# Kernel tuning notes

Hardware: AMD Instinct MI355X
Metric: run time of the kernel (lower is better)

## Reference

```python
import jax, jax.numpy as jnp
import numpy as np

EPS = 1e-6
DELTA = 1e-6
GAMMA = 1.0


def setup_inputs() -> dict:
    key = jax.random.key(0)
    ks = jax.random.split(key, 6)
    B, N, D, DDIR, DSIM = 2, 384, 256, 128, 64
    sc = lambda d: 1.0 / np.sqrt(d)
    return {
        "t": jax.random.normal(ks[0], (B, N, D), jnp.float32),
        "Qd": jax.random.normal(ks[1], (D, DDIR), jnp.float32) * sc(D),
        "Kd": jax.random.normal(ks[2], (D, DDIR), jnp.float32) * sc(D),
        "Vd": jax.random.normal(ks[3], (DDIR, D), jnp.float32) * sc(DDIR),
        "Qs": jax.random.normal(ks[4], (D, DSIM), jnp.float32) * sc(D),
        "Ks": jax.random.normal(ks[5], (D, DSIM), jnp.float32) * sc(D),
        "a_l": jnp.ones((1,), jnp.float32),
        "b_l": jnp.zeros((1,), jnp.float32),
    }


def reference(t, Qd, Kd, Vd, Qs, Ks, a_l, b_l):
    B, N, D = t.shape
    d_sim = Qs.shape[1]
    # --- similarity: s_ij = <Qs t_i, Ks t_j>/sqrt(d_sim), then symmetrize ---
    q = t @ Qs  # (B,N,d_sim)
    k = t @ Ks
    s = jnp.einsum('bnd,bmd->bnm', q, k) / jnp.sqrt(jnp.float32(d_sim))
    s = 0.5 * (s + s.transpose(0, 2, 1))
    # --- global z-score over off-diagonal entries (biased var) ---
    eye = jnp.eye(N, dtype=bool)[None]  # (1,N,N)
    cnt = jnp.float32(N * (N - 1))
    mu = jnp.where(eye, 0.0, s).sum((1, 2), keepdims=True) / cnt  # (B,1,1)
    var = jnp.where(eye, 0.0, (s - mu) ** 2).sum((1, 2), keepdims=True) / cnt
    s_hat = (s - mu) / jnp.sqrt(var + EPS)
    tilde_s = a_l.reshape(-1, 1, 1) * s_hat + b_l.reshape(-1, 1, 1)
    # --- gates / mass / inertia / apportioned step ---
    A = jax.nn.sigmoid(tilde_s)                                  # (B,N,N)
    m = 1.0 / (jnp.exp(GAMMA * tilde_s).sum(axis=2) + EPS)       # (B,N)
    w = A * m[:, None, :]                                        # w_ij = m_j A_ij
    alpha = A * (w / (w.sum(axis=2, keepdims=True) + DELTA))     # (B,N,N)
    # --- antisymmetric Hadamard direction gate ---
    qd = t @ Qd  # (B,N,d_dir)
    kd = t @ Kd
    had = qd[:, :, None, :] * kd[:, None, :, :]                  # (B,N,N,d_dir)
    kappa = jnp.einsum('bijr,rd->bijd', had, Vd)                 # (B,N,N,D)
    gate = jax.nn.sigmoid(kappa - kappa.transpose(0, 2, 1, 3))
    Dpair = gate * (t[:, :, None, :] - t[:, None, :, :])         # D_ij = gate*(t_i - t_j)
    # --- exclude self pairs, aggregate update ---
    off = ~eye  # (1,N,N)
    alpha = jnp.where(off, alpha, 0.0)
    Dpair = jnp.where(off[..., None], Dpair, 0.0)
    t_next = t - jnp.einsum('bnm,bnmd->bnd', alpha, Dpair)
    return t_next
```

## Files before the change

### kernel.cpp

```cpp
#include <hip/hip_runtime.h>

#define Bn 2
#define Nn 384
#define Dn 256
#define Rn 128
#define Sn 64
#define BNn (Bn*Nn)
#define NEG_LOG2E -1.44269504088896f

typedef short short8 __attribute__((ext_vector_type(8)));
typedef float f32x4 __attribute__((ext_vector_type(4)));
typedef unsigned int uint;
typedef unsigned short ushort;

static __device__ __forceinline__ float fast_sigmoid(float x) {
    return __builtin_amdgcn_rcpf(1.0f + __expf(-x));
}
static __device__ __forceinline__ ushort f2bf(float f) {
    uint u = __float_as_uint(f);
    uint r = (u + 0x7fffu + ((u >> 16) & 1u)) >> 16;
    return (ushort)r;
}
static __device__ __forceinline__ float bf2f(ushort u) {
    return __uint_as_float(((uint)u) << 16);
}

__global__ __launch_bounds__(256)
void prep_kernel(const float* __restrict__ t,
                 const float* __restrict__ Qd, const float* __restrict__ Kd,
                 const float* __restrict__ Vd,
                 const float* __restrict__ Qs, const float* __restrict__ Ks,
                 float* __restrict__ q, float* __restrict__ k,
                 ushort* __restrict__ qdb, ushort* __restrict__ kdb,
                 ushort* __restrict__ VdT, float* __restrict__ stats) {
    const int bi = blockIdx.x;
    const int tid = threadIdx.x;
    if (bi >= BNn) {
        const int idx = (bi - BNn) * 256 + tid;
        const int d = idx >> 7, r = idx & 127;
        VdT[idx] = f2bf(NEG_LOG2E * Vd[(size_t)r * Dn + d]);
        if (bi == BNn && tid < 4) stats[tid] = 0.0f;
        return;
    }
    __shared__ float trow[Dn];
    trow[tid] = t[(size_t)bi * Dn + tid];
    __syncthreads();
    {
        const float* W = (tid < 128) ? Qd : Kd;
        ushort* ob = (tid < 128) ? qdb : kdb;
        const int col = tid & 127;
        float a0 = 0.f;
        for (int kk = 0; kk < Dn; kk += 4) {
            float4 tv = *(const float4*)&trow[kk];
            a0 += tv.x * W[(size_t)(kk + 0) * 128 + col]
                + tv.y * W[(size_t)(kk + 1) * 128 + col]
                + tv.z * W[(size_t)(kk + 2) * 128 + col]
                + tv.w * W[(size_t)(kk + 3) * 128 + col];
        }
        ob[(size_t)bi * 128 + col] = f2bf(a0);
    }
    if (tid < 128) {
        const float* W = (tid < 64) ? Qs : Ks;
        float* of = (tid < 64) ? q : k;
        const int col = tid & 63;
        float a0 = 0.f;
        for (int kk = 0; kk < Dn; kk += 4) {
            float4 tv = *(const float4*)&trow[kk];
            a0 += tv.x * W[(size_t)(kk + 0) * 64 + col]
                + tv.y * W[(size_t)(kk + 1) * 64 + col]
                + tv.z * W[(size_t)(kk + 2) * 64 + col]
                + tv.w * W[(size_t)(kk + 3) * 64 + col];
        }
        of[(size_t)bi * 64 + col] = a0;
    }
}

__global__ __launch_bounds__(256)
void ssym_kernel(const float* __restrict__ q, const float* __restrict__ k,
                 float* __restrict__ ssym, float* __restrict__ stats) {
    __shared__ float qi[16][68], ki[16][68], qj[16][68], kj[16][68];
    __shared__ float part[8];
    const int b = blockIdx.z, it = blockIdx.x, jt = blockIdx.y;
    const int tid = threadIdx.x;
    const int r0 = tid >> 6, c = tid & 63;
#pragma unroll
    for (int p = 0; p < 4; ++p) {
        int row = r0 + 4 * p;
        qi[row][c] = q[((size_t)(b * Nn + it * 16 + row)) * Sn + c];
        ki[row][c] = k[((size_t)(b * Nn + it * 16 + row)) * Sn + c];
        qj[row][c] = q[((size_t)(b * Nn + jt * 16 + row)) * Sn + c];
        kj[row][c] = k[((size_t)(b * Nn + jt * 16 + row)) * Sn + c];
    }
    __syncthreads();
    const int ti = tid >> 4, tj = tid & 15;
    float acc = 0.0f;
#pragma unroll
    for (int dd = 0; dd < Sn; dd += 4) {
        float4 a  = *(const float4*)&qi[ti][dd];
        float4 bb = *(const float4*)&kj[tj][dd];
        float4 cc = *(const float4*)&qj[tj][dd];
        float4 d  = *(const float4*)&ki[ti][dd];
        acc += a.x * bb.x + a.y * bb.y + a.z * bb.z + a.w * bb.w
             + cc.x * d.x + cc.y * d.y + cc.z * d.z + cc.w * d.w;
    }
    const float sval = acc * 0.0625f;
    const int gi = it * 16 + ti, gj = jt * 16 + tj;
    ssym[((size_t)(b * Nn + gi)) * Nn + gj] = sval;
    const float v = (gi == gj) ? 0.0f : sval;

    float vs = v, v2 = v * v;
#pragma unroll
    for (int mask = 32; mask > 0; mask >>= 1) {
        vs += __shfl_xor(vs, mask);
        v2 += __shfl_xor(v2, mask);
    }
    const int lane = tid & 63, wave = tid >> 6;
    if (lane == 0) { part[wave] = vs; part[4 + wave] = v2; }
    __syncthreads();
    if (tid == 0) {
        atomicAdd(&stats[b * 2 + 0], part[0] + part[1] + part[2] + part[3]);
        atomicAdd(&stats[b * 2 + 1], part[4] + part[5] + part[6] + part[7]);
    }
}

__global__ __launch_bounds__(256)
void m_kernel(const float* __restrict__ ssym, const float* __restrict__ stats,
              const float* __restrict__ a_l, const float* __restrict__ b_l,
              float* __restrict__ m) {
    __shared__ float part[4];
    const int row = blockIdx.x;
    const int b = row / Nn;
    const float cnt_inv = 1.0f / (float)(Nn * (Nn - 1));
    const float mu = stats[b * 2 + 0] * cnt_inv;
    const float var = stats[b * 2 + 1] * cnt_inv - mu * mu;
    const float isg = rsqrtf(var + 1e-6f);
    const float a = a_l[0], bbias = b_l[0];
    const int tid = threadIdx.x;
    float sum = __expf(a * (ssym[(size_t)row * Nn + tid] - mu) * isg + bbias);
    if (tid < 128)
        sum += __expf(a * (ssym[(size_t)row * Nn + 256 + tid] - mu) * isg + bbias);
#pragma unroll
    for (int mask = 32; mask > 0; mask >>= 1) sum += __shfl_xor(sum, mask);
    if ((tid & 63) == 0) part[tid >> 6] = sum;
    __syncthreads();
    if (tid == 0) m[row] = 1.0f / (part[0] + part[1] + part[2] + part[3] + 1e-6f);
}

__global__ __launch_bounds__(256, 4)
void pair_kernel(const float* __restrict__ t, const float* __restrict__ ssym,
                 const float* __restrict__ mptr, const float* __restrict__ stats,
                 const float* __restrict__ a_l, const float* __restrict__ b_l,
                 const ushort* __restrict__ qdb, const ushort* __restrict__ kdb,
                 const ushort* __restrict__ VdT, float* __restrict__ out) {
    __shared__ ushort qs_lds[2][4096];
    __shared__ ushort ks_lds[2][4096];
    __shared__ float alpha_s[Nn];
    __shared__ float part[4];

    const int blk = blockIdx.x;
    const int bi = blk >> 2;
    const int dq = blk & 3;
    const int b = bi / Nn;
    const int i = bi - b * Nn;
    const int tid = threadIdx.x;
    const int wave = tid >> 6, lane = tid & 63;
    const int ln = lane & 15, quad = lane >> 4;
    const int wd0 = dq * 64 + wave * 16;

    {
        const float cnt_inv = 1.0f / (float)(Nn * (Nn - 1));
        const float mu = stats[b * 2 + 0] * cnt_inv;
        const float var = stats[b * 2 + 1] * cnt_inv - mu * mu;
        const float isg = rsqrtf(var + 1e-6f);
        const float a = a_l[0], bbias = b_l[0];
        float A0, am0, A1 = 0.f, am1 = 0.f;
        {
            float s0 = ssym[(size_t)bi * Nn + tid];
            A0 = fast_sigmoid(a * (s0 - mu) * isg + bbias);
            am0 = A0 * mptr[b * Nn + tid];
        }
        if (tid < 128) {
            float s1 = ssym[(size_t)bi * Nn + 256 + tid];
            A1 = fast_sigmoid(a * (s1 - mu) * isg + bbias);
            am1 = A1 * mptr[b * Nn + 256 + tid];
        }
        float sum = am0 + am1;
#pragma unroll
        for (int mask = 32; mask > 0; mask >>= 1) sum += __shfl_xor(sum, mask);
        if (lane == 0) part[wave] = sum;
        __syncthreads();
        const float inv = 1.0f / (part[0] + part[1] + part[2] + part[3] + 1e-6f);
        alpha_s[tid] = (tid == i) ? 0.f : A0 * am0 * inv;
        if (tid < 128)
            alpha_s[256 + tid] = ((256 + tid) == i) ? 0.f : A1 * am1 * inv;
    }

    short8 uf[4], wf[4];
    {
        const size_t qrow = (size_t)bi * Rn;
#pragma unroll
        for (int ks = 0; ks < 4; ++ks) {
            short8 qv = *(const short8*)&qdb[qrow + ks * 32 + quad * 8];
            short8 kv = *(const short8*)&kdb[qrow + ks * 32 + quad * 8];
            short8 vv = *(const short8*)&VdT[(size_t)(wd0 + ln) * Rn + ks * 32 + quad * 8];
            short8 uu, ww;
#pragma unroll
            for (int e = 0; e < 8; ++e) {
                float vf_ = bf2f((ushort)vv[e]);
                uu[e] = (short)f2bf(vf_ * bf2f((ushort)qv[e]));
                ww[e] = (short)f2bf(vf_ * bf2f((ushort)kv[e]));
            }
            uf[ks] = uu;
            wf[ks] = ww;
        }
    }

    float4 tiv = *(const float4*)&t[(size_t)bi * Dn + wd0 + quad * 4];
    float4 outac = make_float4(0.f, 0.f, 0.f, 0.f);

    const ushort* qsrc = qdb + (size_t)b * Nn * Rn;
    const ushort* ksrc = kdb + (size_t)b * Nn * Rn;
    const float* tbase_ = t + (size_t)b * Nn * Dn + wd0 + quad * 4;

    const int jr = tid >> 4;
    const int ch = tid & 15;
    const int wb = (ch >> 2) * 1024 + (ch & 3) * 256 + ((jr ^ (ch & 7)) * 16);

    uint4 sq0, sq1, sk0, sk1;

    {
        const ushort* q0 = qsrc + (size_t)jr * Rn + ch * 8;
        const ushort* k0 = ksrc + (size_t)jr * Rn + ch * 8;
        sq0 = *(const uint4*)q0;  sq1 = *(const uint4*)(q0 + 16 * Rn);
        sk0 = *(const uint4*)k0;  sk1 = *(const uint4*)(k0 + 16 * Rn);
        *(uint4*)((char*)&qs_lds[0][0] + wb)        = sq0;
        *(uint4*)((char*)&qs_lds[0][0] + wb + 4096) = sq1;
        *(uint4*)((char*)&ks_lds[0][0] + wb)        = sk0;
        *(uint4*)((char*)&ks_lds[0][0] + wb + 4096) = sk1;
    }
    __syncthreads();

    const int lane_off = ((ln ^ quad) * 16) + quad * 256;

    float4 tj_cur = *(const float4*)&tbase_[(size_t)ln * Dn];

    int cur = 0;
#pragma unroll 1
    for (int tt = 0; tt < Nn / 32; ++tt) {
        const int tn = (tt + 1 < Nn / 32) ? tt + 1 : 0;
        {
            const ushort* q0 = qsrc + (size_t)(tn * 32 + jr) * Rn + ch * 8;
            const ushort* k0 = ksrc + (size_t)(tn * 32 + jr) * Rn + ch * 8;
            sq0 = *(const uint4*)q0;  sq1 = *(const uint4*)(q0 + 16 * Rn);
            sk0 = *(const uint4*)k0;  sk1 = *(const uint4*)(k0 + 16 * Rn);
        }

        const char* qbuf = (const char*)&qs_lds[cur][0];
        const char* kbuf = (const char*)&ks_lds[cur][0];

#pragma unroll
        for (int s = 0; s < 2; ++s) {
            const int jj = tt * 2 + s;
            const int jn = (jj + 1 < Nn / 16) ? jj + 1 : 0;
            float4 tj_nxt = *(const float4*)&tbase_[(size_t)(jn * 16 + ln) * Dn];

            f32x4 accU = {0.f, 0.f, 0.f, 0.f}, accW = {0.f, 0.f, 0.f, 0.f};
#pragma unroll
            for (int ks = 0; ks < 4; ++ks) {
                const int off = s * 4096 + ks * 1024 + (lane_off ^ ((ks & 1) << 6));
                short8 bk = *(const short8*)(kbuf + off);
                short8 bq = *(const short8*)(qbuf + off);
                accU = __builtin_amdgcn_mfma_f32_16x16x32_bf16(uf[ks], bk, accU, 0, 0, 0);
                accW = __builtin_amdgcn_mfma_f32_16x16x32_bf16(wf[ks], bq, accW, 0, 0, 0);
            }
            const float al = alpha_s[jj * 16 + ln];
            float e0 = accU[0] - accW[0];
            float e1 = accU[1] - accW[1];
            float e2 = accU[2] - accW[2];
            float e3 = accU[3] - accW[3];
            float g0 = __builtin_amdgcn_rcpf(1.0f + __builtin_amdgcn_exp2f(e0));
            float g1 = __builtin_amdgcn_rcpf(1.0f + __builtin_amdgcn_exp2f(e1));
            float g2 = __builtin_amdgcn_rcpf(1.0f + __builtin_amdgcn_exp2f(e2));
            float g3 = __builtin_amdgcn_rcpf(1.0f + __builtin_amdgcn_exp2f(e3));
            outac.x += al * g0 * (tiv.x - tj_cur.x);
            outac.y += al * g1 * (tiv.y - tj_cur.y);
            outac.z += al * g2 * (tiv.z - tj_cur.z);
            outac.w += al * g3 * (tiv.w - tj_cur.w);
            tj_cur = tj_nxt;
        }

        {
            char* qd_ = (char*)&qs_lds[cur ^ 1][0];
            char* kd_ = (char*)&ks_lds[cur ^ 1][0];
            *(uint4*)(qd_ + wb)        = sq0;
            *(uint4*)(qd_ + wb + 4096) = sq1;
            *(uint4*)(kd_ + wb)        = sk0;
            *(uint4*)(kd_ + wb + 4096) = sk1;
        }
        __syncthreads();
        cur ^= 1;
    }

    {
        float4 v = outac;
#pragma unroll
        for (int mask = 1; mask < 16; mask <<= 1) {
            v.x += __shfl_xor(v.x, mask);
            v.y += __shfl_xor(v.y, mask);
            v.z += __shfl_xor(v.z, mask);
            v.w += __shfl_xor(v.w, mask);
        }
        if (ln == 0) {
            float4 o;
            o.x = tiv.x - v.x;
            o.y = tiv.y - v.y;
            o.z = tiv.z - v.z;
            o.w = tiv.w - v.w;
            *(float4*)&out[(size_t)bi * Dn + wd0 + quad * 4] = o;
        }
    }
}

extern "C" void kernel_launch(void* const* d_in, const int* in_sizes, int n_in,
                              void* d_out, int out_size, void* d_ws, size_t ws_size,
                              hipStream_t stream) {
    const float* t   = (const float*)d_in[0];
    const float* Qd  = (const float*)d_in[1];
    const float* Kd  = (const float*)d_in[2];
    const float* Vd  = (const float*)d_in[3];
    const float* Qs  = (const float*)d_in[4];
    const float* Ks  = (const float*)d_in[5];
    const float* a_l = (const float*)d_in[6];
    const float* b_l = (const float*)d_in[7];
    float* out = (float*)d_out;
    float* ws  = (float*)d_ws;

    float* q     = ws;
    float* k     = q + BNn * Sn;
    float* ssym  = k + BNn * Sn;
    float* m     = ssym + (size_t)BNn * Nn;
    float* stats = m + BNn;
    ushort* qdb  = (ushort*)(stats + 8);
    ushort* kdb  = qdb + (size_t)BNn * Rn;
    ushort* VdT  = kdb + (size_t)BNn * Rn;

    hipLaunchKernelGGL(prep_kernel, dim3(BNn + 128), dim3(256), 0, stream,
                       t, Qd, Kd, Vd, Qs, Ks, q, k, qdb, kdb, VdT, stats);
    hipLaunchKernelGGL(ssym_kernel, dim3(Nn / 16, Nn / 16, Bn), dim3(256), 0, stream,
                       q, k, ssym, stats);
    hipLaunchKernelGGL(m_kernel, dim3(BNn), dim3(256), 0, stream, ssym, stats, a_l, b_l, m);
    hipLaunchKernelGGL(pair_kernel, dim3(BNn * 4), dim3(256), 0, stream,
                       t, ssym, m, stats, a_l, b_l, qdb, kdb, VdT, out);
}
```

Before: 186.3 us.

## Use 512-thread pair blocks covering half of D per row

```diff
diff --git a/kernel.cpp b/kernel.cpp
--- a/kernel.cpp
+++ b/kernel.cpp
@@ -146,7 +146,7 @@
     if (tid == 0) m[row] = 1.0f / (part[0] + part[1] + part[2] + part[3] + 1e-6f);
 }
 
-__global__ __launch_bounds__(256, 4)
+__global__ __launch_bounds__(512, 4)
 void pair_kernel(const float* __restrict__ t, const float* __restrict__ ssym,
                  const float* __restrict__ mptr, const float* __restrict__ stats,
                  const float* __restrict__ a_l, const float* __restrict__ b_l,
@@ -155,17 +155,17 @@
     __shared__ ushort qs_lds[2][4096];
     __shared__ ushort ks_lds[2][4096];
     __shared__ float alpha_s[Nn];
-    __shared__ float part[4];
+    __shared__ float part[8];
 
     const int blk = blockIdx.x;
-    const int bi = blk >> 2;
-    const int dq = blk & 3;
+    const int bi = blk >> 1;
+    const int dh = blk & 1;
     const int b = bi / Nn;
     const int i = bi - b * Nn;
     const int tid = threadIdx.x;
     const int wave = tid >> 6, lane = tid & 63;
     const int ln = lane & 15, quad = lane >> 4;
-    const int wd0 = dq * 64 + wave * 16;
+    const int wd0 = dh * 128 + wave * 16;
 
     {
         const float cnt_inv = 1.0f / (float)(Nn * (Nn - 1));
@@ -173,26 +173,22 @@
         const float var = stats[b * 2 + 1] * cnt_inv - mu * mu;
         const float isg = rsqrtf(var + 1e-6f);
         const float a = a_l[0], bbias = b_l[0];
-        float A0, am0, A1 = 0.f, am1 = 0.f;
-        {
+        float A0 = 0.f, am0 = 0.f;
+        if (tid < Nn) {
             float s0 = ssym[(size_t)bi * Nn + tid];
             A0 = fast_sigmoid(a * (s0 - mu) * isg + bbias);
             am0 = A0 * mptr[b * Nn + tid];
         }
-        if (tid < 128) {
-            float s1 = ssym[(size_t)bi * Nn + 256 + tid];
-            A1 = fast_sigmoid(a * (s1 - mu) * isg + bbias);
-            am1 = A1 * mptr[b * Nn + 256 + tid];
-        }
-        float sum = am0 + am1;
+        float sum = am0;
 #pragma unroll
         for (int mask = 32; mask > 0; mask >>= 1) sum += __shfl_xor(sum, mask);
         if (lane == 0) part[wave] = sum;
         __syncthreads();
-        const float inv = 1.0f / (part[0] + part[1] + part[2] + part[3] + 1e-6f);
-        alpha_s[tid] = (tid == i) ? 0.f : A0 * am0 * inv;
-        if (tid < 128)
-            alpha_s[256 + tid] = ((256 + tid) == i) ? 0.f : A1 * am1 * inv;
+        const float tot = part[0] + part[1] + part[2] + part[3]
+                        + part[4] + part[5] + part[6] + part[7];
+        const float inv = 1.0f / (tot + 1e-6f);
+        if (tid < Nn)
+            alpha_s[tid] = (tid == i) ? 0.f : A0 * am0 * inv;
     }
 
     short8 uf[4], wf[4];
@@ -224,19 +220,18 @@
 
     const int jr = tid >> 4;
     const int ch = tid & 15;
-    const int wb = (ch >> 2) * 1024 + (ch & 3) * 256 + ((jr ^ (ch & 7)) * 16);
-
-    uint4 sq0, sq1, sk0, sk1;
+    const int wb = (jr >> 4) * 4096 + (ch >> 2) * 1024 + (ch & 3) * 256
+                 + (((jr & 15) ^ (ch & 7)) * 16);
+
+    uint4 sq, sk;
 
     {
         const ushort* q0 = qsrc + (size_t)jr * Rn + ch * 8;
         const ushort* k0 = ksrc + (size_t)jr * Rn + ch * 8;
-        sq0 = *(const uint4*)q0;  sq1 = *(const uint4*)(q0 + 16 * Rn);
-        sk0 = *(const uint4*)k0;  sk1 = *(const uint4*)(k0 + 16 * Rn);
-        *(uint4*)((char*)&qs_lds[0][0] + wb)        = sq0;
-        *(uint4*)((char*)&qs_lds[0][0] + wb + 4096) = sq1;
-        *(uint4*)((char*)&ks_lds[0][0] + wb)        = sk0;
-        *(uint4*)((char*)&ks_lds[0][0] + wb + 4096) = sk1;
+        sq = *(const uint4*)q0;
+        sk = *(const uint4*)k0;
+        *(uint4*)((char*)&qs_lds[0][0] + wb) = sq;
+        *(uint4*)((char*)&ks_lds[0][0] + wb) = sk;
     }
     __syncthreads();
 
@@ -251,8 +246,8 @@
         {
             const ushort* q0 = qsrc + (size_t)(tn * 32 + jr) * Rn + ch * 8;
             const ushort* k0 = ksrc + (size_t)(tn * 32 + jr) * Rn + ch * 8;
-            sq0 = *(const uint4*)q0;  sq1 = *(const uint4*)(q0 + 16 * Rn);
-            sk0 = *(const uint4*)k0;  sk1 = *(const uint4*)(k0 + 16 * Rn);
+            sq = *(const uint4*)q0;
+            sk = *(const uint4*)k0;
         }
 
         const char* qbuf = (const char*)&qs_lds[cur][0];
@@ -290,12 +285,8 @@
         }
 
         {
-            char* qd_ = (char*)&qs_lds[cur ^ 1][0];
-            char* kd_ = (char*)&ks_lds[cur ^ 1][0];
-            *(uint4*)(qd_ + wb)        = sq0;
-            *(uint4*)(qd_ + wb + 4096) = sq1;
-            *(uint4*)(kd_ + wb)        = sk0;
-            *(uint4*)(kd_ + wb + 4096) = sk1;
+            *(uint4*)((char*)&qs_lds[cur ^ 1][0] + wb) = sq;
+            *(uint4*)((char*)&ks_lds[cur ^ 1][0] + wb) = sk;
         }
         __syncthreads();
         cur ^= 1;
@@ -349,6 +340,6 @@
     hipLaunchKernelGGL(ssym_kernel, dim3(Nn / 16, Nn / 16, Bn), dim3(256), 0, stream,
                        q, k, ssym, stats);
     hipLaunchKernelGGL(m_kernel, dim3(BNn), dim3(256), 0, stream, ssym, stats, a_l, b_l, m);
-    hipLaunchKernelGGL(pair_kernel, dim3(BNn * 4), dim3(256), 0, stream,
+    hipLaunchKernelGGL(pair_kernel, dim3(BNn * 2), dim3(512), 0, stream,
                        t, ssym, m, stats, a_l, b_l, qdb, kdb, VdT, out);
 }
```

New measurement: 180.9 us, median of 2. 1.03x faster.
